# Optimization experiments

Measured on AMD Instinct MI355X. Metric: run time of the kernel, lower is better.

## Reference

```python
import jax, jax.numpy as jnp
import numpy as np

N = 8192      # total nodes (32 graphs x 256 nodes)
B = 32        # graphs in batch
E = 65536     # edges per graph (avg degree 16)
DK = 512      # d_k = d_v
H = 32        # mlp / conv channel width
VB = 2048     # body visual dim
VF = 512      # face visual dim
EPS = 1e-5


def setup_inputs() -> dict:
    key = jax.random.key(0)
    ks = jax.random.split(key, 26)
    def n(k, sh, s=1.0):
        return jax.random.normal(k, sh, dtype=jnp.float32) * s
    s2, s512, s32 = 1.0 / np.sqrt(2.0), 1.0 / np.sqrt(512.0), 1.0 / np.sqrt(32.0)
    inp = {}
    inp["x"] = n(ks[0], (N, 2))
    inp["visual_body"] = n(ks[1], (N, VB))
    inp["visual_face"] = n(ks[2], (N, VF))
    # attention projections (no bias)
    inp["Wq"] = n(ks[3], (2, DK), s2)
    inp["Wk"] = n(ks[4], (2, DK), s2)
    inp["Wv"] = n(ks[5], (2, DK), s2)
    # input_mlp: LayerNorm(512) -> PReLU -> Linear(512,32)
    inp["ln_g"] = jnp.ones((DK,), jnp.float32)
    inp["ln_b"] = jnp.zeros((DK,), jnp.float32)
    inp["prelu_a"] = jnp.float32(0.25)
    inp["mlp_W"] = n(ks[6], (DK, H), s512)
    inp["mlp_b"] = jnp.zeros((H,), jnp.float32)
    # node projection Linear(32,1)
    inp["np_W"] = n(ks[7], (H, 1), s32)
    inp["np_b"] = jnp.zeros((1,), jnp.float32)
    # CMCosConv linear weights (32->32) for body / face
    inp["body_W"] = n(ks[8], (H, H), s32)
    inp["body_b"] = jnp.zeros((H,), jnp.float32)
    inp["face_W"] = n(ks[9], (H, H), s32)
    inp["face_b"] = jnp.zeros((H,), jnp.float32)
    # gcn projections Linear(32,1)
    inp["pb_W"] = n(ks[10], (H, 1), s32)
    inp["pb_b"] = jnp.zeros((1,), jnp.float32)
    inp["pf_W"] = n(ks[11], (H, 1), s32)
    inp["pf_b"] = jnp.zeros((1,), jnp.float32)
    # int-valued graph structure
    inp["edge_index_body"] = jax.random.randint(ks[12], (2, E), 0, N)
    inp["edge_index_face"] = jax.random.randint(ks[13], (2, E), 0, N)
    inp["batch_vec"] = jnp.arange(N, dtype=jnp.int64) // (N // B)  # 32 graphs, 256 nodes each
    return inp


def cmcos_conv(x, edge_index, visual, W, b):
    # per-edge cosine(visual_src, visual_dst) * Linear(x_src), scatter-sum to dst
    src, dst = edge_index[0], edge_index[1]
    h = x @ W + b                                          # [N, H]
    vn = visual * jax.lax.rsqrt(jnp.sum(visual * visual, -1, keepdims=True) + 1e-8)
    w = jnp.sum(vn[src] * vn[dst], axis=-1)                # [E] cosine edge weights
    msg = w[:, None] * h[src]                              # [E, H]
    return jax.ops.segment_sum(msg, dst, num_segments=x.shape[0])


def reference(x, visual_body, visual_face, Wq, Wk, Wv, ln_g, ln_b, prelu_a,
              mlp_W, mlp_b, np_W, np_b, body_W, body_b, face_W, face_b,
              pb_W, pb_b, pf_W, pf_b, edge_index_body, edge_index_face, batch_vec):
    sz_b = int(batch_vec[-1]) + 1
    q = (x @ Wq).reshape(sz_b, -1, DK)
    k = (x @ Wk).reshape(sz_b, -1, DK)
    v = (x @ Wv).reshape(sz_b, -1, DK)
    attn = jax.nn.softmax(jnp.einsum('bqd,bkd->bqk', q, k) / np.sqrt(DK), axis=-1)
    out = jnp.einsum('bqk,bkd->bqd', attn, v).reshape(-1, DK)   # [N, 512]
    # input_mlp: LayerNorm -> PReLU -> Linear (dropout is identity in eval)
    mu = jnp.mean(out, -1, keepdims=True)
    var = jnp.mean((out - mu) ** 2, -1, keepdims=True)
    h = (out - mu) * jax.lax.rsqrt(var + EPS) * ln_g + ln_b
    h = jnp.where(h >= 0, h, prelu_a * h)
    h = h @ mlp_W + mlp_b                                       # [N, 32]
    nodes_scores = (h @ np_W + np_b)[:, 0]
    hb = cmcos_conv(h, edge_index_body, visual_body, body_W, body_b)
    hf = cmcos_conv(h, edge_index_face, visual_face, face_W, face_b)
    gcn_scores_body = (hb @ pb_W + pb_b)[:, 0]
    gcn_scores_face = (hf @ pf_W + pf_b)[:, 0]
    return nodes_scores + gcn_scores_body + gcn_scores_face
```

## Files before the change

### kernel.cpp

```cpp
#include <hip/hip_runtime.h>

#define NN 8192
#define NB 32
#define NG 256
#define NE 65536
#define DK 512
#define HC 32
#define DB 2048
#define DF 512

#define BODY_DW (NN*DB/4)
#define FACE_DW (NN*DF/4)
#define B_BODY (BODY_DW/2048)
#define B_FACE (FACE_DW/2048)
#define QSCALE 16.0f

typedef float v4f __attribute__((ext_vector_type(4)));

#if __has_builtin(__builtin_amdgcn_sdot4)
#define HW_SDOT 1
#else
#define HW_SDOT 0
#endif

__device__ __forceinline__ unsigned pack4_i8(float4 v) {
    int i0 = (int)rintf(fmaxf(fminf(v.x * QSCALE, 127.f), -127.f));
    int i1 = (int)rintf(fmaxf(fminf(v.y * QSCALE, 127.f), -127.f));
    int i2 = (int)rintf(fmaxf(fminf(v.z * QSCALE, 127.f), -127.f));
    int i3 = (int)rintf(fmaxf(fminf(v.w * QSCALE, 127.f), -127.f));
    return (unsigned)(i0 & 255) | ((unsigned)(i1 & 255) << 8)
         | ((unsigned)(i2 & 255) << 16) | ((unsigned)(i3 & 255) << 24);
}
__device__ __forceinline__ int sdot4(int a, int b, int c) {
#if HW_SDOT
    return __builtin_amdgcn_sdot4(a, b, c, false);
#else
    c += (int)(signed char)(a)       * (int)(signed char)(b);
    c += (int)(signed char)(a >> 8)  * (int)(signed char)(b >> 8);
    c += (int)(signed char)(a >> 16) * (int)(signed char)(b >> 16);
    c += (int)(signed char)(a >> 24) * (int)(signed char)(b >> 24);
    return c;
#endif
}
__device__ __forceinline__ int dot16(int4 a, int4 b, int c) {
    c = sdot4(a.x, b.x, c);
    c = sdot4(a.y, b.y, c);
    c = sdot4(a.z, b.z, c);
    c = sdot4(a.w, b.w, c);
    return c;
}
__device__ __forceinline__ float d4(float4 v) {
    return v.x*v.x + v.y*v.y + v.z*v.z + v.w*v.w;
}
__device__ __forceinline__ v4f prelu4(v4f nd, float alpha) {
    v4f r;
    r.x = (nd.x >= 0.f) ? nd.x : alpha*nd.x;
    r.y = (nd.y >= 0.f) ? nd.y : alpha*nd.y;
    r.z = (nd.z >= 0.f) ? nd.z : alpha*nd.z;
    r.w = (nd.w >= 0.f) ? nd.w : alpha*nd.w;
    return r;
}

struct Params {
    const float *vb, *vf, *x, *Wq, *Wk, *Wv, *ln_g, *ln_b, *prelu_a;
    const float *mlp_W, *mlp_b, *np_W, *np_b, *body_W, *body_b, *face_W, *face_b;
    const float *pb_W, *pb_b, *pf_W, *pf_b;
    const int *eib, *eif;
    unsigned *vnb, *vnf;
    float *invb, *invf;
    float *a_ws, *sb, *sf, *fused;
    float *mvec;
    float *out;
};

__global__ __launch_bounds__(256) void k1_kernel(Params p) {
    __shared__ float2 xs[NG];
    __shared__ float pm[4][4];
    __shared__ float sm4[4];
    __shared__ float rss[16];
    __shared__ float wred[4][8];
    __shared__ float fs_np[HC], fs_fb[HC], fs_ff[HC];
    const int bid = blockIdx.x, tid = threadIdx.x;
    const int lane = tid & 63, wave = tid >> 6;

    if (bid < NB) {
        const int gg = bid;
        xs[tid] = ((const float2*)p.x)[gg*NG + tid];
        const int d = tid * 2;
        float q0a = p.Wq[d],    q0b = p.Wq[d+1];
        float q1a = p.Wq[DK+d], q1b = p.Wq[DK+d+1];
        float k0a = p.Wk[d],    k0b = p.Wk[d+1];
        float k1a = p.Wk[DK+d], k1b = p.Wk[DK+d+1];
        float m00 = q0a*k0a + q0b*k0b;
        float m01 = q0a*k1a + q0b*k1b;
        float m10 = q1a*k0a + q1b*k0b;
        float m11 = q1a*k1a + q1b*k1b;
        #pragma unroll
        for (int off = 32; off > 0; off >>= 1) {
            m00 += __shfl_down(m00,off); m01 += __shfl_down(m01,off);
            m10 += __shfl_down(m10,off); m11 += __shfl_down(m11,off);
        }
        if (lane == 0) { pm[wave][0]=m00; pm[wave][1]=m01; pm[wave][2]=m10; pm[wave][3]=m11; }
        __syncthreads();
        if (tid < 4) sm4[tid] = pm[0][tid] + pm[1][tid] + pm[2][tid] + pm[3][tid];
        __syncthreads();
        const float scale = 0.04419417382415922f;
        const float2 xi = xs[tid];
        const float u0 = (xi.x*sm4[0] + xi.y*sm4[2]) * scale;
        const float u1 = (xi.x*sm4[1] + xi.y*sm4[3]) * scale;
        float m = -1e30f;
        for (int j = 0; j < NG; j++) m = fmaxf(m, u0*xs[j].x + u1*xs[j].y);
        float S = 0.f, a0 = 0.f, a1 = 0.f;
        for (int j = 0; j < NG; j++) {
            float2 xj = xs[j];
            float pr = __expf(u0*xj.x + u1*xj.y - m);
            S += pr; a0 += pr*xj.x; a1 += pr*xj.y;
        }
        const float invS = 1.f / S;
        ((float2*)p.a_ws)[gg*NG + tid] = make_float2(a0*invS, a1*invS);
        return;
    }
    if (bid == NB) {
        {
            const int d = tid * 2;
            float u0 = p.Wv[d], u1 = p.Wv[d+1];
            float w0 = p.Wv[DK+d], w1 = p.Wv[DK+d+1];
            float s0 = u0 + u1, s1 = w0 + w1;
            float q00 = u0*u0 + u1*u1, q01 = u0*w0 + u1*w1, q11 = w0*w0 + w1*w1;
            #pragma unroll
            for (int off = 1; off < 64; off <<= 1) {
                s0 += __shfl_xor(s0,off); s1 += __shfl_xor(s1,off);
                q00 += __shfl_xor(q00,off); q01 += __shfl_xor(q01,off); q11 += __shfl_xor(q11,off);
            }
            if (lane == 0) {
                wred[wave][0]=s0; wred[wave][1]=s1; wred[wave][2]=q00; wred[wave][3]=q01; wred[wave][4]=q11;
            }
        }
        if (tid < HC) {
            float sB = 0.f, sF = 0.f;
            #pragma unroll 8
            for (int c = 0; c < HC; c++) {
                sB += p.body_W[tid*HC + c] * p.pb_W[c];
                sF += p.face_W[tid*HC + c] * p.pf_W[c];
            }
            fs_fb[tid] = sB; fs_ff[tid] = sF;
            fs_np[tid] = p.np_W[tid];
        } else if (tid == HC) {
            float s = 0.f;
            for (int c = 0; c < HC; c++) s += p.body_b[c] * p.pb_W[c];
            p.fused[64] = s;
        } else if (tid == HC + 1) {
            float s = 0.f;
            for (int c = 0; c < HC; c++) s += p.face_b[c] * p.pf_W[c];
            p.fused[65] = s;
        }
        __syncthreads();
        if (tid < 5) p.fused[66+tid] = wred[0][tid]+wred[1][tid]+wred[2][tid]+wred[3][tid];
        #pragma unroll
        for (int rr = tid; rr < DK; rr += 256) {
            const float* row = p.mlp_W + rr*HC;
            float dnp = 0.f, db = 0.f, df = 0.f;
            #pragma unroll 8
            for (int c = 0; c < HC; c++) {
                float w = row[c];
                dnp += w * fs_np[c]; db += w * fs_fb[c]; df += w * fs_ff[c];
            }
            p.mvec[rr] = dnp; p.mvec[DK + rr] = db; p.mvec[2*DK + rr] = df;
        }
        if (tid < 3) {
            const float* fv = (tid == 0) ? fs_np : (tid == 1) ? fs_fb : fs_ff;
            float s = 0.f;
            for (int c = 0; c < HC; c++) s += p.mlp_b[c] * fv[c];
            p.mvec[3*DK + tid] = s;
        }
        return;
    }
    {
        const int pb = bid - (NB + 1);
        const bool body = pb < B_BODY;
        const float4* __restrict__ src = body ? (const float4*)p.vb : (const float4*)p.vf;
        unsigned* __restrict__ dst = body ? p.vnb : p.vnf;
        const int base = (body ? pb : pb - B_BODY) * 2048 + tid;
        if (tid < 16) rss[tid] = 0.f;
        __syncthreads();
        float4 v0 = src[base];
        float4 v1 = src[base + 256];
        float4 v2 = src[base + 512];
        float4 v3 = src[base + 768];
        float4 v4 = src[base + 1024];
        float4 v5 = src[base + 1280];
        float4 v6 = src[base + 1536];
        float4 v7 = src[base + 1792];
        __builtin_amdgcn_sched_barrier(0);
        dst[base]        = pack4_i8(v0);
        dst[base + 256]  = pack4_i8(v1);
        dst[base + 512]  = pack4_i8(v2);
        dst[base + 768]  = pack4_i8(v3);
        dst[base + 1024] = pack4_i8(v4);
        dst[base + 1280] = pack4_i8(v5);
        dst[base + 1536] = pack4_i8(v6);
        dst[base + 1792] = pack4_i8(v7);
        if (body) {
            float sq[4];
            sq[0] = d4(v0) + d4(v1);
            sq[1] = d4(v2) + d4(v3);
            sq[2] = d4(v4) + d4(v5);
            sq[3] = d4(v6) + d4(v7);
            #pragma unroll
            for (int r = 0; r < 4; r++) {
                float ss = sq[r];
                #pragma unroll
                for (int off = 32; off > 0; off >>= 1) ss += __shfl_xor(ss, off);
                if (lane == 0) atomicAdd(&rss[r], ss);
            }
            __syncthreads();
            if (tid < 4) p.invb[pb*4 + tid] = rsqrtf(rss[tid] + 1e-8f);
        } else {
            float sq[8] = {d4(v0), d4(v1), d4(v2), d4(v3), d4(v4), d4(v5), d4(v6), d4(v7)};
            #pragma unroll
            for (int j = 0; j < 8; j++) {
                float ss = sq[j];
                #pragma unroll
                for (int off = 32; off > 0; off >>= 1) ss += __shfl_xor(ss, off);
                if (lane == 0) atomicAdd(&rss[(wave >> 1) + 2*j], ss);
            }
            __syncthreads();
            if (tid < 16) p.invf[(pb - B_BODY)*16 + tid] = rsqrtf(rss[tid] + 1e-8f);
        }
    }
}

__global__ __launch_bounds__(256) void k2_kernel(Params p) {
    const int tid = threadIdx.x;
    const int wave = tid >> 6, lane = tid & 63;
    const int node = blockIdx.x * 4 + wave;

    const float a0 = p.a_ws[node*2], a1 = p.a_ws[node*2+1];
    const float s0 = p.fused[66], s1 = p.fused[67];
    const float q00 = p.fused[68], q01 = p.fused[69], q11 = p.fused[70];
    const float mean = (a0*s0 + a1*s1) * (1.f/DK);
    const float msq  = (a0*a0*q00 + 2.f*a0*a1*q01 + a1*a1*q11) * (1.f/DK);
    const float inv  = rsqrtf(msq - mean*mean + 1e-5f);
    const float alpha = p.prelu_a[0];

    const v4f* wv0 = (const v4f*)p.Wv;
    const v4f* wv1 = (const v4f*)(p.Wv + DK);
    const v4f* g4 = (const v4f*)p.ln_g;
    const v4f* b4 = (const v4f*)p.ln_b;
    const v4f* mnp = (const v4f*)p.mvec;
    const v4f* mb  = (const v4f*)(p.mvec + DK);
    const v4f* mf  = (const v4f*)(p.mvec + 2*DK);

    const int c4 = lane * 2;
    v4f t0 = prelu4((a0*wv0[c4]   + a1*wv1[c4]   - mean) * inv * g4[c4]   + b4[c4],   alpha);
    v4f t1 = prelu4((a0*wv0[c4+1] + a1*wv1[c4+1] - mean) * inv * g4[c4+1] + b4[c4+1], alpha);

    v4f q0 = t0*mnp[c4] + t1*mnp[c4+1];
    v4f q1 = t0*mb[c4]  + t1*mb[c4+1];
    v4f q2 = t0*mf[c4]  + t1*mf[c4+1];
    float d0 = (q0.x+q0.y) + (q0.z+q0.w);
    float d1 = (q1.x+q1.y) + (q1.z+q1.w);
    float d2 = (q2.x+q2.y) + (q2.z+q2.w);
    #pragma unroll
    for (int off = 1; off < 64; off <<= 1) {
        d0 += __shfl_xor(d0, off);
        d1 += __shfl_xor(d1, off);
        d2 += __shfl_xor(d2, off);
    }
    if (lane == 0) {
        const float qinv2 = 1.0f / (QSCALE * QSCALE);
        p.out[node] = d0 + p.mvec[3*DK] + p.np_b[0] + p.pb_b[0] + p.pf_b[0];
        p.sb[node] = (d1 + p.mvec[3*DK+1] + p.fused[64]) * qinv2;
        p.sf[node] = (d2 + p.mvec[3*DK+2] + p.fused[65]) * qinv2;
    }
}

__global__ __launch_bounds__(256) void scat_kernel(Params p) {
    const int wave = threadIdx.x >> 6, lane = threadIdx.x & 63;
    if (blockIdx.x < NE/8) {
        const int e = blockIdx.x * 8 + wave * 2;
        const int sA = p.eib[e],     dA = p.eib[NE + e];
        const int sB = p.eib[e + 1], dB = p.eib[NE + e + 1];
        const int4* A0 = (const int4*)(p.vnb + (size_t)sA * (DB/4));
        const int4* B0 = (const int4*)(p.vnb + (size_t)dA * (DB/4));
        const int4* A1 = (const int4*)(p.vnb + (size_t)sB * (DB/4));
        const int4* B1 = (const int4*)(p.vnb + (size_t)dB * (DB/4));
        int4 a00 = A0[lane], a01 = A0[lane + 64];
        int4 b00 = B0[lane], b01 = B0[lane + 64];
        int4 a10 = A1[lane], a11 = A1[lane + 64];
        int4 b10 = B1[lane], b11 = B1[lane + 64];
        int x0 = dot16(a01, b01, dot16(a00, b00, 0));
        int x1 = dot16(a11, b11, dot16(a10, b10, 0));
        #pragma unroll
        for (int off = 1; off < 64; off <<= 1) {
            x0 += __shfl_xor(x0, off);
            x1 += __shfl_xor(x1, off);
        }
        if (lane == 0) {
            atomicAdd(&p.out[dA], (float)x0 * p.invb[sA] * p.invb[dA] * p.sb[sA]);
            atomicAdd(&p.out[dB], (float)x1 * p.invb[sB] * p.invb[dB] * p.sb[sB]);
        }
    } else {
        const int e = (blockIdx.x - NE/8) * 16 + wave * 4;
        const int s0 = p.eif[e],     d0 = p.eif[NE + e];
        const int s1 = p.eif[e + 1], d1 = p.eif[NE + e + 1];
        const int s2 = p.eif[e + 2], d2 = p.eif[NE + e + 2];
        const int s3 = p.eif[e + 3], d3 = p.eif[NE + e + 3];
        const int2* ap0 = (const int2*)(p.vnf + (size_t)s0 * (DF/4));
        const int2* bp0 = (const int2*)(p.vnf + (size_t)d0 * (DF/4));
        const int2* ap1 = (const int2*)(p.vnf + (size_t)s1 * (DF/4));
        const int2* bp1 = (const int2*)(p.vnf + (size_t)d1 * (DF/4));
        const int2* ap2 = (const int2*)(p.vnf + (size_t)s2 * (DF/4));
        const int2* bp2 = (const int2*)(p.vnf + (size_t)d2 * (DF/4));
        const int2* ap3 = (const int2*)(p.vnf + (size_t)s3 * (DF/4));
        const int2* bp3 = (const int2*)(p.vnf + (size_t)d3 * (DF/4));
        int2 a0 = ap0[lane], b0 = bp0[lane];
        int2 a1 = ap1[lane], b1 = bp1[lane];
        int2 a2 = ap2[lane], b2 = bp2[lane];
        int2 a3 = ap3[lane], b3 = bp3[lane];
        int x0 = sdot4(a0.y, b0.y, sdot4(a0.x, b0.x, 0));
        int x1 = sdot4(a1.y, b1.y, sdot4(a1.x, b1.x, 0));
        int x2 = sdot4(a2.y, b2.y, sdot4(a2.x, b2.x, 0));
        int x3 = sdot4(a3.y, b3.y, sdot4(a3.x, b3.x, 0));
        #pragma unroll
        for (int off = 1; off < 64; off <<= 1) {
            x0 += __shfl_xor(x0, off);
            x1 += __shfl_xor(x1, off);
            x2 += __shfl_xor(x2, off);
            x3 += __shfl_xor(x3, off);
        }
        if (lane == 0) {
            atomicAdd(&p.out[d0], (float)x0 * p.invf[s0] * p.invf[d0] * p.sf[s0]);
            atomicAdd(&p.out[d1], (float)x1 * p.invf[s1] * p.invf[d1] * p.sf[s1]);
            atomicAdd(&p.out[d2], (float)x2 * p.invf[s2] * p.invf[d2] * p.sf[s2]);
            atomicAdd(&p.out[d3], (float)x3 * p.invf[s3] * p.invf[d3] * p.sf[s3]);
        }
    }
}

extern "C" void kernel_launch(void* const* d_in, const int* in_sizes, int n_in,
                              void* d_out, int out_size, void* d_ws, size_t ws_size,
                              hipStream_t stream) {
    char* ws = (char*)d_ws;
    size_t off = 0;
    auto alloc = [&](size_t bytes) { void* pp = ws + off; off += (bytes + 15) & ~size_t(15); return pp; };

    Params p;
    p.vb      = (const float*)d_in[1];
    p.vf      = (const float*)d_in[2];
    p.x       = (const float*)d_in[0];
    p.Wq      = (const float*)d_in[3];
    p.Wk      = (const float*)d_in[4];
    p.Wv      = (const float*)d_in[5];
    p.ln_g    = (const float*)d_in[6];
    p.ln_b    = (const float*)d_in[7];
    p.prelu_a = (const float*)d_in[8];
    p.mlp_W   = (const float*)d_in[9];
    p.mlp_b   = (const float*)d_in[10];
    p.np_W    = (const float*)d_in[11];
    p.np_b    = (const float*)d_in[12];
    p.body_W  = (const float*)d_in[13];
    p.body_b  = (const float*)d_in[14];
    p.face_W  = (const float*)d_in[15];
    p.face_b  = (const float*)d_in[16];
    p.pb_W    = (const float*)d_in[17];
    p.pb_b    = (const float*)d_in[18];
    p.pf_W    = (const float*)d_in[19];
    p.pf_b    = (const float*)d_in[20];
    p.eib     = (const int*)d_in[21];
    p.eif     = (const int*)d_in[22];
    p.vnb     = (unsigned*)alloc((size_t)BODY_DW*4);
    p.vnf     = (unsigned*)alloc((size_t)FACE_DW*4);
    p.invb    = (float*)alloc((size_t)NN*4);
    p.invf    = (float*)alloc((size_t)NN*4);
    p.a_ws    = (float*)alloc((size_t)NN*2*4);
    p.sb      = (float*)alloc((size_t)NN*4);
    p.sf      = (float*)alloc((size_t)NN*4);
    p.fused   = (float*)alloc((size_t)72*4);
    p.mvec    = (float*)alloc((size_t)1544*4);
    p.out     = (float*)d_out;

    k1_kernel<<<NB + 1 + B_BODY + B_FACE, 256, 0, stream>>>(p);
    k2_kernel<<<NN/4, 256, 0, stream>>>(p);
    scat_kernel<<<NE/8 + NE/16, 256, 0, stream>>>(p);
}
```

Baseline: 197.7 us.

## Build destination CSR and gather edges per node instead of per-edge atomics

```diff
diff --git a/kernel.cpp b/kernel.cpp
--- a/kernel.cpp
+++ b/kernel.cpp
@@ -13,6 +13,7 @@
 #define FACE_DW (NN*DF/4)
 #define B_BODY (BODY_DW/2048)
 #define B_FACE (FACE_DW/2048)
+#define B_CNT  512
 #define QSCALE 16.0f
 
 typedef float v4f __attribute__((ext_vector_type(4)));
@@ -68,8 +69,9 @@
     const int *eib, *eif;
     unsigned *vnb, *vnf;
     float *invb, *invf;
-    float *a_ws, *sb, *sf, *fused;
+    float *a_ws, *cb, *cf, *fused;
     float *mvec;
+    int *counts, *starts, *cursor, *esrc;
     float *out;
 };
 
@@ -175,8 +177,14 @@
         }
         return;
     }
+    if (bid < NB + 1 + B_CNT) {
+        const int e = (bid - (NB + 1)) * 256 + tid;
+        if (e < NE) atomicAdd(&p.counts[p.eib[NE + e]], 1);
+        else        atomicAdd(&p.counts[NN + p.eif[e]], 1);
+        return;
+    }
     {
-        const int pb = bid - (NB + 1);
+        const int pb = bid - (NB + 1 + B_CNT);
         const bool body = pb < B_BODY;
         const float4* __restrict__ src = body ? (const float4*)p.vb : (const float4*)p.vf;
         unsigned* __restrict__ dst = body ? p.vnb : p.vnf;
@@ -231,10 +239,36 @@
 }
 
 __global__ __launch_bounds__(256) void k2_kernel(Params p) {
-    const int tid = threadIdx.x;
+    __shared__ int part[256];
+    const int bid = blockIdx.x, tid = threadIdx.x;
     const int wave = tid >> 6, lane = tid & 63;
-    const int node = blockIdx.x * 4 + wave;
-
+
+    if (bid < 2) {
+        const int cbase = bid * NN;
+        const int sbase = bid * (NN + 1);
+        int loc[32];
+        int sum = 0;
+        #pragma unroll
+        for (int j = 0; j < 32; j++) { loc[j] = p.counts[cbase + tid*32 + j]; sum += loc[j]; }
+        part[tid] = sum;
+        __syncthreads();
+        for (int off = 1; off < 256; off <<= 1) {
+            int v = (tid >= off) ? part[tid - off] : 0;
+            __syncthreads();
+            part[tid] += v;
+            __syncthreads();
+        }
+        int run = (tid == 0) ? 0 : part[tid - 1];
+        #pragma unroll
+        for (int j = 0; j < 32; j++) {
+            p.starts[sbase + tid*32 + j] = run;
+            p.cursor[cbase + tid*32 + j] = run;
+            run += loc[j];
+        }
+        if (tid == 255) p.starts[sbase + NN] = run;
+        return;
+    }
+    const int node = (bid - 2) * 4 + wave;
     const float a0 = p.a_ws[node*2], a1 = p.a_ws[node*2+1];
     const float s0 = p.fused[66], s1 = p.fused[67];
     const float q00 = p.fused[68], q01 = p.fused[69], q11 = p.fused[70];
@@ -270,71 +304,88 @@
     if (lane == 0) {
         const float qinv2 = 1.0f / (QSCALE * QSCALE);
         p.out[node] = d0 + p.mvec[3*DK] + p.np_b[0] + p.pb_b[0] + p.pf_b[0];
-        p.sb[node] = (d1 + p.mvec[3*DK+1] + p.fused[64]) * qinv2;
-        p.sf[node] = (d2 + p.mvec[3*DK+2] + p.fused[65]) * qinv2;
+        p.cb[node] = (d1 + p.mvec[3*DK+1] + p.fused[64]) * qinv2 * p.invb[node];
+        p.cf[node] = (d2 + p.mvec[3*DK+2] + p.fused[65]) * qinv2 * p.invf[node];
+    }
+}
+
+__global__ __launch_bounds__(256) void fill_kernel(Params p) {
+    const int e = blockIdx.x * 256 + threadIdx.x;
+    if (e < NE) {
+        int s = p.eib[e], d = p.eib[NE + e];
+        int pos = atomicAdd(&p.cursor[d], 1);
+        p.esrc[pos] = s;
+    } else {
+        int e2 = e - NE;
+        int s = p.eif[e2], d = p.eif[NE + e2];
+        int pos = atomicAdd(&p.cursor[NN + d], 1);
+        p.esrc[NE + pos] = s;
     }
 }
 
 __global__ __launch_bounds__(256) void scat_kernel(Params p) {
     const int wave = threadIdx.x >> 6, lane = threadIdx.x & 63;
-    if (blockIdx.x < NE/8) {
-        const int e = blockIdx.x * 8 + wave * 2;
-        const int sA = p.eib[e],     dA = p.eib[NE + e];
-        const int sB = p.eib[e + 1], dB = p.eib[NE + e + 1];
-        const int4* A0 = (const int4*)(p.vnb + (size_t)sA * (DB/4));
-        const int4* B0 = (const int4*)(p.vnb + (size_t)dA * (DB/4));
-        const int4* A1 = (const int4*)(p.vnb + (size_t)sB * (DB/4));
-        const int4* B1 = (const int4*)(p.vnb + (size_t)dB * (DB/4));
-        int4 a00 = A0[lane], a01 = A0[lane + 64];
-        int4 b00 = B0[lane], b01 = B0[lane + 64];
-        int4 a10 = A1[lane], a11 = A1[lane + 64];
-        int4 b10 = B1[lane], b11 = B1[lane + 64];
-        int x0 = dot16(a01, b01, dot16(a00, b00, 0));
-        int x1 = dot16(a11, b11, dot16(a10, b10, 0));
-        #pragma unroll
-        for (int off = 1; off < 64; off <<= 1) {
-            x0 += __shfl_xor(x0, off);
-            x1 += __shfl_xor(x1, off);
-        }
-        if (lane == 0) {
-            atomicAdd(&p.out[dA], (float)x0 * p.invb[sA] * p.invb[dA] * p.sb[sA]);
-            atomicAdd(&p.out[dB], (float)x1 * p.invb[sB] * p.invb[dB] * p.sb[sB]);
-        }
+    const bool body = blockIdx.x < NN/4;
+    const int node = (body ? blockIdx.x : blockIdx.x - NN/4) * 4 + wave;
+    const int sbase = body ? 0 : (NN + 1);
+    const int s0 = p.starts[sbase + node], s1 = p.starts[sbase + node + 1];
+    float acc = 0.f;
+    if (body) {
+        const int4* D = (const int4*)(p.vnb + (size_t)node * (DB/4));
+        int4 d0 = D[lane], d1 = D[lane + 64];
+        int i = s0;
+        if (i < s1) {
+            int s = p.esrc[i];
+            const int4* A = (const int4*)(p.vnb + (size_t)s * (DB/4));
+            int4 a0 = A[lane], a1 = A[lane + 64];
+            float c = p.cb[s];
+            int4 b0 = d0, b1 = d1; float c2 = 0.f;
+            while (true) {
+                const int i2 = i + 1;
+                const bool more = i2 < s1;
+                if (more) {
+                    int sn = p.esrc[i2];
+                    const int4* A2 = (const int4*)(p.vnb + (size_t)sn * (DB/4));
+                    b0 = A2[lane]; b1 = A2[lane + 64];
+                    c2 = p.cb[sn];
+                }
+                int x = dot16(a1, d1, dot16(a0, d0, 0));
+                acc += (float)x * c;
+                if (!more) break;
+                a0 = b0; a1 = b1; c = c2; i = i2;
+            }
+        }
+        #pragma unroll
+        for (int off = 1; off < 64; off <<= 1) acc += __shfl_xor(acc, off);
+        if (lane == 0) atomicAdd(&p.out[node], acc * p.invb[node]);
     } else {
-        const int e = (blockIdx.x - NE/8) * 16 + wave * 4;
-        const int s0 = p.eif[e],     d0 = p.eif[NE + e];
-        const int s1 = p.eif[e + 1], d1 = p.eif[NE + e + 1];
-        const int s2 = p.eif[e + 2], d2 = p.eif[NE + e + 2];
-        const int s3 = p.eif[e + 3], d3 = p.eif[NE + e + 3];
-        const int2* ap0 = (const int2*)(p.vnf + (size_t)s0 * (DF/4));
-        const int2* bp0 = (const int2*)(p.vnf + (size_t)d0 * (DF/4));
-        const int2* ap1 = (const int2*)(p.vnf + (size_t)s1 * (DF/4));
-        const int2* bp1 = (const int2*)(p.vnf + (size_t)d1 * (DF/4));
-        const int2* ap2 = (const int2*)(p.vnf + (size_t)s2 * (DF/4));
-        const int2* bp2 = (const int2*)(p.vnf + (size_t)d2 * (DF/4));
-        const int2* ap3 = (const int2*)(p.vnf + (size_t)s3 * (DF/4));
-        const int2* bp3 = (const int2*)(p.vnf + (size_t)d3 * (DF/4));
-        int2 a0 = ap0[lane], b0 = bp0[lane];
-        int2 a1 = ap1[lane], b1 = bp1[lane];
-        int2 a2 = ap2[lane], b2 = bp2[lane];
-        int2 a3 = ap3[lane], b3 = bp3[lane];
-        int x0 = sdot4(a0.y, b0.y, sdot4(a0.x, b0.x, 0));
-        int x1 = sdot4(a1.y, b1.y, sdot4(a1.x, b1.x, 0));
-        int x2 = sdot4(a2.y, b2.y, sdot4(a2.x, b2.x, 0));
-        int x3 = sdot4(a3.y, b3.y, sdot4(a3.x, b3.x, 0));
-        #pragma unroll
-        for (int off = 1; off < 64; off <<= 1) {
-            x0 += __shfl_xor(x0, off);
-            x1 += __shfl_xor(x1, off);
-            x2 += __shfl_xor(x2, off);
-            x3 += __shfl_xor(x3, off);
-        }
-        if (lane == 0) {
-            atomicAdd(&p.out[d0], (float)x0 * p.invf[s0] * p.invf[d0] * p.sf[s0]);
-            atomicAdd(&p.out[d1], (float)x1 * p.invf[s1] * p.invf[d1] * p.sf[s1]);
-            atomicAdd(&p.out[d2], (float)x2 * p.invf[s2] * p.invf[d2] * p.sf[s2]);
-            atomicAdd(&p.out[d3], (float)x3 * p.invf[s3] * p.invf[d3] * p.sf[s3]);
-        }
+        const int2* D = (const int2*)(p.vnf + (size_t)node * (DF/4));
+        int2 dd = D[lane];
+        int i = s0;
+        if (i < s1) {
+            int s = p.esrc[NE + i];
+            const int2* A = (const int2*)(p.vnf + (size_t)s * (DF/4));
+            int2 a = A[lane];
+            float c = p.cf[s];
+            int2 b = dd; float c2 = 0.f;
+            while (true) {
+                const int i2 = i + 1;
+                const bool more = i2 < s1;
+                if (more) {
+                    int sn = p.esrc[NE + i2];
+                    const int2* A2 = (const int2*)(p.vnf + (size_t)sn * (DF/4));
+                    b = A2[lane];
+                    c2 = p.cf[sn];
+                }
+                int x = sdot4(a.y, dd.y, sdot4(a.x, dd.x, 0));
+                acc += (float)x * c;
+                if (!more) break;
+                a = b; c = c2; i = i2;
+            }
+        }
+        #pragma unroll
+        for (int off = 1; off < 64; off <<= 1) acc += __shfl_xor(acc, off);
+        if (lane == 0) atomicAdd(&p.out[node], acc * p.invf[node]);
     }
 }
 
@@ -374,13 +425,19 @@
     p.invb    = (float*)alloc((size_t)NN*4);
     p.invf    = (float*)alloc((size_t)NN*4);
     p.a_ws    = (float*)alloc((size_t)NN*2*4);
-    p.sb      = (float*)alloc((size_t)NN*4);
-    p.sf      = (float*)alloc((size_t)NN*4);
+    p.cb      = (float*)alloc((size_t)NN*4);
+    p.cf      = (float*)alloc((size_t)NN*4);
     p.fused   = (float*)alloc((size_t)72*4);
     p.mvec    = (float*)alloc((size_t)1544*4);
+    p.counts  = (int*)alloc((size_t)2*NN*4);
+    p.starts  = (int*)alloc((size_t)2*(NN+1)*4);
+    p.cursor  = (int*)alloc((size_t)2*NN*4);
+    p.esrc    = (int*)alloc((size_t)2*NE*4);
     p.out     = (float*)d_out;
 
-    k1_kernel<<<NB + 1 + B_BODY + B_FACE, 256, 0, stream>>>(p);
-    k2_kernel<<<NN/4, 256, 0, stream>>>(p);
-    scat_kernel<<<NE/8 + NE/16, 256, 0, stream>>>(p);
-}
+    hipMemsetAsync(p.counts, 0, (size_t)2*NN*4, stream);
+    k1_kernel<<<NB + 1 + B_CNT + B_BODY + B_FACE, 256, 0, stream>>>(p);
+    k2_kernel<<<2 + NN/4, 256, 0, stream>>>(p);
+    fill_kernel<<<(2*NE)/256, 256, 0, stream>>>(p);
+    scat_kernel<<<NN/2, 256, 0, stream>>>(p);
+}
```

Result: slower. 208.4 us (+5.4%).

## Bucket edges by destination and gather per node instead of per-edge atomics

Applied to the files above, without the earlier changes.

```diff
diff --git a/kernel.cpp b/kernel.cpp
--- a/kernel.cpp
+++ b/kernel.cpp
@@ -13,6 +13,8 @@
 #define FACE_DW (NN*DF/4)
 #define B_BODY (BODY_DW/2048)
 #define B_FACE (FACE_DW/2048)
+#define B_FILL 512
+#define SLOTS  40
 #define QSCALE 16.0f
 
 typedef float v4f __attribute__((ext_vector_type(4)));
@@ -68,8 +70,9 @@
     const int *eib, *eif;
     unsigned *vnb, *vnf;
     float *invb, *invf;
-    float *a_ws, *sb, *sf, *fused;
+    float *a_ws, *cb, *cf, *fused;
     float *mvec;
+    int *counts, *bkt;
     float *out;
 };
 
@@ -175,8 +178,22 @@
         }
         return;
     }
+    if (bid < NB + 1 + B_FILL) {
+        const int e = (bid - (NB + 1)) * 256 + tid;
+        if (e < NE) {
+            int s = p.eib[e], d = p.eib[NE + e];
+            int slot = atomicAdd(&p.counts[d], 1);
+            if (slot < SLOTS) p.bkt[d*SLOTS + slot] = s;
+        } else {
+            int e2 = e - NE;
+            int s = p.eif[e2], d = p.eif[NE + e2];
+            int slot = atomicAdd(&p.counts[NN + d], 1);
+            if (slot < SLOTS) p.bkt[(NN + d)*SLOTS + slot] = s;
+        }
+        return;
+    }
     {
-        const int pb = bid - (NB + 1);
+        const int pb = bid - (NB + 1 + B_FILL);
         const bool body = pb < B_BODY;
         const float4* __restrict__ src = body ? (const float4*)p.vb : (const float4*)p.vf;
         unsigned* __restrict__ dst = body ? p.vnb : p.vnf;
@@ -270,71 +287,80 @@
     if (lane == 0) {
         const float qinv2 = 1.0f / (QSCALE * QSCALE);
         p.out[node] = d0 + p.mvec[3*DK] + p.np_b[0] + p.pb_b[0] + p.pf_b[0];
-        p.sb[node] = (d1 + p.mvec[3*DK+1] + p.fused[64]) * qinv2;
-        p.sf[node] = (d2 + p.mvec[3*DK+2] + p.fused[65]) * qinv2;
+        p.cb[node] = (d1 + p.mvec[3*DK+1] + p.fused[64]) * qinv2 * p.invb[node];
+        p.cf[node] = (d2 + p.mvec[3*DK+2] + p.fused[65]) * qinv2 * p.invf[node];
     }
 }
 
 __global__ __launch_bounds__(256) void scat_kernel(Params p) {
     const int wave = threadIdx.x >> 6, lane = threadIdx.x & 63;
-    if (blockIdx.x < NE/8) {
-        const int e = blockIdx.x * 8 + wave * 2;
-        const int sA = p.eib[e],     dA = p.eib[NE + e];
-        const int sB = p.eib[e + 1], dB = p.eib[NE + e + 1];
-        const int4* A0 = (const int4*)(p.vnb + (size_t)sA * (DB/4));
-        const int4* B0 = (const int4*)(p.vnb + (size_t)dA * (DB/4));
-        const int4* A1 = (const int4*)(p.vnb + (size_t)sB * (DB/4));
-        const int4* B1 = (const int4*)(p.vnb + (size_t)dB * (DB/4));
-        int4 a00 = A0[lane], a01 = A0[lane + 64];
-        int4 b00 = B0[lane], b01 = B0[lane + 64];
-        int4 a10 = A1[lane], a11 = A1[lane + 64];
-        int4 b10 = B1[lane], b11 = B1[lane + 64];
-        int x0 = dot16(a01, b01, dot16(a00, b00, 0));
-        int x1 = dot16(a11, b11, dot16(a10, b10, 0));
+    const bool body = blockIdx.x < NN/4;
+    const int node = (body ? blockIdx.x : blockIdx.x - NN/4) * 4 + wave;
+    float acc = 0.f;
+    if (body) {
+        const int cnt = min(p.counts[node], SLOTS);
+        const int* bkt = p.bkt + node*SLOTS;
+        const int4* D = (const int4*)(p.vnb + (size_t)node * (DB/4));
+        int4 d0 = D[lane], d1 = D[lane + 64];
+        for (int i = 0; i < cnt; i += 4) {
+            const int sA = bkt[i];
+            const int sB = (i+1 < cnt) ? bkt[i+1] : node;
+            const int sC = (i+2 < cnt) ? bkt[i+2] : node;
+            const int sD = (i+3 < cnt) ? bkt[i+3] : node;
+            const float cA = p.cb[sA];
+            const float cB = (i+1 < cnt) ? p.cb[sB] : 0.f;
+            const float cC = (i+2 < cnt) ? p.cb[sC] : 0.f;
+            const float cD = (i+3 < cnt) ? p.cb[sD] : 0.f;
+            const int4* A0 = (const int4*)(p.vnb + (size_t)sA * (DB/4));
+            const int4* A1 = (const int4*)(p.vnb + (size_t)sB * (DB/4));
+            const int4* A2 = (const int4*)(p.vnb + (size_t)sC * (DB/4));
+            const int4* A3 = (const int4*)(p.vnb + (size_t)sD * (DB/4));
+            int4 a00 = A0[lane], a01 = A0[lane + 64];
+            int4 a10 = A1[lane], a11 = A1[lane + 64];
+            int4 a20 = A2[lane], a21 = A2[lane + 64];
+            int4 a30 = A3[lane], a31 = A3[lane + 64];
+            __builtin_amdgcn_sched_barrier(0);
+            int x0 = dot16(a01, d1, dot16(a00, d0, 0));
+            int x1 = dot16(a11, d1, dot16(a10, d0, 0));
+            int x2 = dot16(a21, d1, dot16(a20, d0, 0));
+            int x3 = dot16(a31, d1, dot16(a30, d0, 0));
+            acc += (float)x0*cA + (float)x1*cB + (float)x2*cC + (float)x3*cD;
+        }
         #pragma unroll
-        for (int off = 1; off < 64; off <<= 1) {
-            x0 += __shfl_xor(x0, off);
-            x1 += __shfl_xor(x1, off);
-        }
-        if (lane == 0) {
-            atomicAdd(&p.out[dA], (float)x0 * p.invb[sA] * p.invb[dA] * p.sb[sA]);
-            atomicAdd(&p.out[dB], (float)x1 * p.invb[sB] * p.invb[dB] * p.sb[sB]);
-        }
+        for (int off = 1; off < 64; off <<= 1) acc += __shfl_xor(acc, off);
+        if (lane == 0) atomicAdd(&p.out[node], acc * p.invb[node]);
     } else {
-        const int e = (blockIdx.x - NE/8) * 16 + wave * 4;
-        const int s0 = p.eif[e],     d0 = p.eif[NE + e];
-        const int s1 = p.eif[e + 1], d1 = p.eif[NE + e + 1];
-        const int s2 = p.eif[e + 2], d2 = p.eif[NE + e + 2];
-        const int s3 = p.eif[e + 3], d3 = p.eif[NE + e + 3];
-        const int2* ap0 = (const int2*)(p.vnf + (size_t)s0 * (DF/4));
-        const int2* bp0 = (const int2*)(p.vnf + (size_t)d0 * (DF/4));
-        const int2* ap1 = (const int2*)(p.vnf + (size_t)s1 * (DF/4));
-        const int2* bp1 = (const int2*)(p.vnf + (size_t)d1 * (DF/4));
-        const int2* ap2 = (const int2*)(p.vnf + (size_t)s2 * (DF/4));
-        const int2* bp2 = (const int2*)(p.vnf + (size_t)d2 * (DF/4));
-        const int2* ap3 = (const int2*)(p.vnf + (size_t)s3 * (DF/4));
-        const int2* bp3 = (const int2*)(p.vnf + (size_t)d3 * (DF/4));
-        int2 a0 = ap0[lane], b0 = bp0[lane];
-        int2 a1 = ap1[lane], b1 = bp1[lane];
-        int2 a2 = ap2[lane], b2 = bp2[lane];
-        int2 a3 = ap3[lane], b3 = bp3[lane];
-        int x0 = sdot4(a0.y, b0.y, sdot4(a0.x, b0.x, 0));
-        int x1 = sdot4(a1.y, b1.y, sdot4(a1.x, b1.x, 0));
-        int x2 = sdot4(a2.y, b2.y, sdot4(a2.x, b2.x, 0));
-        int x3 = sdot4(a3.y, b3.y, sdot4(a3.x, b3.x, 0));
+        const int cnt = min(p.counts[NN + node], SLOTS);
+        const int* bkt = p.bkt + (size_t)(NN + node)*SLOTS;
+        const int2* D = (const int2*)(p.vnf + (size_t)node * (DF/4));
+        int2 dd = D[lane];
+        for (int i = 0; i < cnt; i += 4) {
+            const int sA = bkt[i];
+            const int sB = (i+1 < cnt) ? bkt[i+1] : node;
+            const int sC = (i+2 < cnt) ? bkt[i+2] : node;
+            const int sD = (i+3 < cnt) ? bkt[i+3] : node;
+            const float cA = p.cf[sA];
+            const float cB = (i+1 < cnt) ? p.cf[sB] : 0.f;
+            const float cC = (i+2 < cnt) ? p.cf[sC] : 0.f;
+            const float cD = (i+3 < cnt) ? p.cf[sD] : 0.f;
+            const int2* A0 = (const int2*)(p.vnf + (size_t)sA * (DF/4));
+            const int2* A1 = (const int2*)(p.vnf + (size_t)sB * (DF/4));
+            const int2* A2 = (const int2*)(p.vnf + (size_t)sC * (DF/4));
+            const int2* A3 = (const int2*)(p.vnf + (size_t)sD * (DF/4));
+            int2 a0 = A0[lane];
+            int2 a1 = A1[lane];
+            int2 a2 = A2[lane];
+            int2 a3 = A3[lane];
+            __builtin_amdgcn_sched_barrier(0);
+            int x0 = sdot4(a0.y, dd.y, sdot4(a0.x, dd.x, 0));
+            int x1 = sdot4(a1.y, dd.y, sdot4(a1.x, dd.x, 0));
+            int x2 = sdot4(a2.y, dd.y, sdot4(a2.x, dd.x, 0));
+            int x3 = sdot4(a3.y, dd.y, sdot4(a3.x, dd.x, 0));
+            acc += (float)x0*cA + (float)x1*cB + (float)x2*cC + (float)x3*cD;
+        }
         #pragma unroll
-        for (int off = 1; off < 64; off <<= 1) {
-            x0 += __shfl_xor(x0, off);
-            x1 += __shfl_xor(x1, off);
-            x2 += __shfl_xor(x2, off);
-            x3 += __shfl_xor(x3, off);
-        }
-        if (lane == 0) {
-            atomicAdd(&p.out[d0], (float)x0 * p.invf[s0] * p.invf[d0] * p.sf[s0]);
-            atomicAdd(&p.out[d1], (float)x1 * p.invf[s1] * p.invf[d1] * p.sf[s1]);
-            atomicAdd(&p.out[d2], (float)x2 * p.invf[s2] * p.invf[d2] * p.sf[s2]);
-            atomicAdd(&p.out[d3], (float)x3 * p.invf[s3] * p.invf[d3] * p.sf[s3]);
-        }
+        for (int off = 1; off < 64; off <<= 1) acc += __shfl_xor(acc, off);
+        if (lane == 0) atomicAdd(&p.out[node], acc * p.invf[node]);
     }
 }
 
@@ -374,13 +400,16 @@
     p.invb    = (float*)alloc((size_t)NN*4);
     p.invf    = (float*)alloc((size_t)NN*4);
     p.a_ws    = (float*)alloc((size_t)NN*2*4);
-    p.sb      = (float*)alloc((size_t)NN*4);
-    p.sf      = (float*)alloc((size_t)NN*4);
+    p.cb      = (float*)alloc((size_t)NN*4);
+    p.cf      = (float*)alloc((size_t)NN*4);
     p.fused   = (float*)alloc((size_t)72*4);
     p.mvec    = (float*)alloc((size_t)1544*4);
+    p.counts  = (int*)alloc((size_t)2*NN*4);
+    p.bkt     = (int*)alloc((size_t)2*NN*SLOTS*4);
     p.out     = (float*)d_out;
 
-    k1_kernel<<<NB + 1 + B_BODY + B_FACE, 256, 0, stream>>>(p);
+    hipMemsetAsync(p.counts, 0, (size_t)2*NN*4, stream);
+    k1_kernel<<<NB + 1 + B_FILL + B_BODY + B_FACE, 256, 0, stream>>>(p);
     k2_kernel<<<NN/4, 256, 0, stream>>>(p);
-    scat_kernel<<<NE/8 + NE/16, 256, 0, stream>>>(p);
-}
+    scat_kernel<<<NN/2, 256, 0, stream>>>(p);
+}
```

Measured after the change: 193.2 us. 1.02x faster.
